# Optimization experiments

Measured on AMD Instinct MI355X. Metric: run time of the kernel, lower is better.

Reference implementation:

```python
import jax, jax.numpy as jnp
import numpy as np

L, M, B = 32768, 8, 8192      # lines, max neighbors per line, blocks
LIN, BIN, H = 768, 768, 512   # line_in_dim, block_in_dim, hidden_size
NH, DH = 8, 512 // 8          # heads, head_dim
LN_EPS = 1e-5


def _ln(x, g, b):
    mu = jnp.mean(x, axis=-1, keepdims=True)
    var = jnp.mean(jnp.square(x - mu), axis=-1, keepdims=True)
    return (x - mu) * jax.lax.rsqrt(var + LN_EPS) * g + b


def setup_inputs() -> dict:
    key = jax.random.key(0)
    ks = jax.random.split(key, 12)
    w = lambda k, shape, fan: jax.random.normal(k, shape, jnp.float32) * (fan ** -0.5)
    return {
        'global_lines': jax.random.normal(ks[0], (L, LIN), jnp.float32),
        'block_reprs': jax.random.normal(ks[1], (B, BIN), jnp.float32),
        'Wq': w(ks[2], (H, LIN), LIN),            # q_proj (no bias)
        'Wkv': w(ks[3], (H, BIN), BIN),           # kv_proj (no bias)
        'qn_g': jnp.ones((H,), jnp.float32), 'qn_b': jnp.zeros((H,), jnp.float32),
        'kvn_g': jnp.ones((H,), jnp.float32), 'kvn_b': jnp.zeros((H,), jnp.float32),
        'in_proj_w': w(ks[4], (3 * H, H), H), 'in_proj_b': jnp.zeros((3 * H,), jnp.float32),
        'out_w': w(ks[5], (H, H), H), 'out_b': jnp.zeros((H,), jnp.float32),
        'p1_w': w(ks[6], (H, 2 * H), 2 * H), 'p1_b': jnp.zeros((H,), jnp.float32),
        'ln1_g': jnp.ones((H,), jnp.float32), 'ln1_b': jnp.zeros((H,), jnp.float32),
        'p2_w': w(ks[7], (H, H), H), 'p2_b': jnp.zeros((H,), jnp.float32),
        'ln2_g': jnp.ones((H,), jnp.float32), 'ln2_b': jnp.zeros((H,), jnp.float32),
        'head_w': w(ks[8], (1, H), H), 'head_b': jnp.zeros((1,), jnp.float32),
        'K_indices': jax.random.randint(ks[9], (L, M), 0, B, jnp.int32),
        'neighbor_counts': jnp.clip(jax.random.randint(ks[10], (L,), 0, M + 1, jnp.int32), 1, M),
    }


def reference(global_lines, block_reprs, Wq, Wkv, qn_g, qn_b, kvn_g, kvn_b,
              in_proj_w, in_proj_b, out_w, out_b,
              p1_w, p1_b, ln1_g, ln1_b, p2_w, p2_b, ln2_g, ln2_b,
              head_w, head_b, K_indices, neighbor_counts):
    # q = LN(q_proj(lines))                              [L, H]
    q = _ln(global_lines @ Wq.T, qn_g, qn_b)
    # gather neighbor block reprs, project, LN           [L, M, H]
    kv = _ln(block_reprs[K_indices] @ Wkv.T, kvn_g, kvn_b)
    pad = jnp.arange(M)[None, :] >= neighbor_counts[:, None]  # True = padded key

    # torch nn.MultiheadAttention with query length 1 per line
    wq_i, wk_i, wv_i = jnp.split(in_proj_w, 3, axis=0)
    bq_i, bk_i, bv_i = jnp.split(in_proj_b, 3, axis=0)
    qh = (q @ wq_i.T + bq_i).reshape(L, NH, DH)
    kh = (kv @ wk_i.T + bk_i).reshape(L, M, NH, DH)
    vh = (kv @ wv_i.T + bv_i).reshape(L, M, NH, DH)
    scores = jnp.einsum('lhd,lmhd->lhm', qh, kh) / np.float32(np.sqrt(DH))
    scores = jnp.where(pad[:, None, :], jnp.finfo(scores.dtype).min, scores)
    attn = jax.nn.softmax(scores, axis=-1)
    ctx = jnp.einsum('lhm,lmhd->lhd', attn, vh).reshape(L, H)
    attn_out = ctx @ out_w.T + out_b

    # line_proj: Linear(2H->H) + LN + GELU + residual(Linear + LN + GELU)
    x = jnp.concatenate([q, attn_out], axis=-1)
    x = jax.nn.gelu(_ln(x @ p1_w.T + p1_b, ln1_g, ln1_b), approximate=False)
    x = x + jax.nn.gelu(_ln(x @ p2_w.T + p2_b, ln2_g, ln2_b), approximate=False)
    logits = (x @ head_w.T + head_b)[:, 0]
    return jax.nn.sigmoid(logits)
```

## Files before the change

### kernel.cpp

```cpp
#include <hip/hip_runtime.h>
#include <math.h>


typedef unsigned short u16;
typedef unsigned int u32;
using bf16x8 = __attribute__((ext_vector_type(8))) __bf16;
using u16x8  = __attribute__((ext_vector_type(8))) u16;
using f32x4  = __attribute__((ext_vector_type(4))) float;

__device__ __forceinline__ u16 f2bf(float f) {
    u32 u = __builtin_bit_cast(u32, f);
    u32 r = u + 0x7fffu + ((u >> 16) & 1u);
    return (u16)(r >> 16);
}
__device__ __forceinline__ float bf2f(u16 h) {
    return __builtin_bit_cast(float, (u32)h << 16);
}
__device__ __forceinline__ float gelu_exact(float x) {
    return 0.5f * x * (1.0f + erff(x * 0.70710678118654752440f));
}

__device__ __forceinline__ float breduce1(float s0, float* sm) {
    #pragma unroll
    for (int off = 32; off > 0; off >>= 1) s0 += __shfl_down(s0, off);
    const int lane = threadIdx.x & 63, w = threadIdx.x >> 6;
    __syncthreads();
    if (lane == 0) sm[w] = s0;
    __syncthreads();
    return sm[0] + sm[1] + sm[2] + sm[3];
}

__global__ __launch_bounds__(256) void cvt_bf16(
    const float* __restrict__ s, u16* __restrict__ d, int n)
{
    const int i = (blockIdx.x * 256 + threadIdx.x) * 4;
    if (i >= n) return;
    const float4 v = *reinterpret_cast<const float4*>(s + i);
    ushort4 o = make_ushort4(f2bf(v.x), f2bf(v.y), f2bf(v.z), f2bf(v.w));
    *reinterpret_cast<ushort4*>(d + i) = o;
}

struct CvtJobs {
    const float* s[5];
    u16* d[5];
    int cum[6];
};
__global__ __launch_bounds__(256) void cvt_multi(CvtJobs j)
{
    const int g = blockIdx.x * 256 + threadIdx.x;
    if (g >= j.cum[5]) return;
    int seg = 0;
    #pragma unroll
    for (int k = 1; k < 5; ++k) seg += (g >= j.cum[k]);
    const int q = g - j.cum[seg];
    const float4 v = *reinterpret_cast<const float4*>(j.s[seg] + q * 4);
    ushort4 o = make_ushort4(f2bf(v.x), f2bf(v.y), f2bf(v.z), f2bf(v.w));
    *reinterpret_cast<ushort4*>(j.d[seg] + q * 4) = o;
}

__global__ __launch_bounds__(256) void fold_w2(
    const float* __restrict__ p1w, const float* __restrict__ outw,
    u16* __restrict__ p1cb)
{
    __shared__ float As[16][65];
    __shared__ float Bs[16][65];
    const int tx = threadIdx.x & 15, ty = threadIdx.x >> 4;
    const int i0 = blockIdx.y * 64, j0 = blockIdx.x * 64;
    const int lr = threadIdx.x >> 2;
    const int lc = (threadIdx.x & 3) * 4;
    const int kr = threadIdx.x >> 4;
    const int jc = (threadIdx.x & 15) * 4;
    float acc[4][4] = {};
    for (int k0 = 0; k0 < 512; k0 += 16) {
        const float4 av = *reinterpret_cast<const float4*>(
            p1w + (size_t)(i0 + lr) * 1024 + 512 + k0 + lc);
        As[lc + 0][lr] = av.x; As[lc + 1][lr] = av.y;
        As[lc + 2][lr] = av.z; As[lc + 3][lr] = av.w;
        const float4 bv = *reinterpret_cast<const float4*>(
            outw + (size_t)(k0 + kr) * 512 + j0 + jc);
        Bs[kr][jc + 0] = bv.x; Bs[kr][jc + 1] = bv.y;
        Bs[kr][jc + 2] = bv.z; Bs[kr][jc + 3] = bv.w;
        __syncthreads();
        #pragma unroll
        for (int kk = 0; kk < 16; ++kk) {
            float a[4], b[4];
            #pragma unroll
            for (int i = 0; i < 4; ++i) a[i] = As[kk][ty * 4 + i];
            #pragma unroll
            for (int jj = 0; jj < 4; ++jj) b[jj] = Bs[kk][tx * 4 + jj];
            #pragma unroll
            for (int i = 0; i < 4; ++i)
                #pragma unroll
                for (int jj = 0; jj < 4; ++jj)
                    acc[i][jj] = fmaf(a[i], b[jj], acc[i][jj]);
        }
        __syncthreads();
    }
    #pragma unroll
    for (int i = 0; i < 4; ++i)
        #pragma unroll
        for (int jj = 0; jj < 4; ++jj)
            p1cb[(size_t)(i0 + ty * 4 + i) * 1024 + 512 + j0 + tx * 4 + jj] =
                f2bf(acc[i][jj]);
}

__global__ __launch_bounds__(64) void fold_bias(
    const float* __restrict__ p1w, const float* __restrict__ outb,
    const float* __restrict__ p1b, float* __restrict__ bias2)
{
    const int i = blockIdx.x, lane = threadIdx.x;
    float s = 0.0f;
    #pragma unroll
    for (int k = lane; k < 512; k += 64)
        s += p1w[(size_t)i * 1024 + 512 + k] * outb[k];
    #pragma unroll
    for (int off = 32; off > 0; off >>= 1) s += __shfl_down(s, off);
    if (lane == 0) bias2[i] = s + p1b[i];
}

template<bool HAS_A2, bool STATS>
__global__ __launch_bounds__(256) void gemm_bf16(
    const u16* __restrict__ A1, const u16* __restrict__ A2, int K1, int K,
    const u16* __restrict__ W, const float* __restrict__ bias,
    u16* __restrict__ C, int N, float* __restrict__ stats)
{
    __shared__ __bf16 As[128 * 32];
    __shared__ __bf16 Ws[128 * 32];
    const int tid = threadIdx.x;
    const int w = tid >> 6, lane = tid & 63;
    const int row0 = blockIdx.y * 128;
    const int col0 = blockIdx.x * 128;
    const int wr = (w >> 1) * 64, wc = (w & 1) * 64;
    const int fr = lane & 15, fg = lane >> 4;

    int srow[2], scol[2], soff[2];
    #pragma unroll
    for (int c = 0; c < 2; ++c) {
        const int bo = w * 2048 + c * 1024 + lane * 16;
        srow[c] = bo >> 6;
        scol[c] = (bo & 63) >> 1;
        soff[c] = (w * 2048 + c * 1024) >> 1;
    }

    f32x4 acc[4][4] = {};

    for (int k0 = 0; k0 < K; k0 += 32) {
        #pragma unroll
        for (int c = 0; c < 2; ++c) {
            const u16* asrc;
            if (HAS_A2) {
                const bool first = (k0 < K1);
                const u16* base = first ? A1 : A2;
                const int ldk = first ? K1 : (K - K1);
                const int kk  = first ? k0 : (k0 - K1);
                asrc = base + (size_t)(row0 + srow[c]) * ldk + kk + scol[c];
            } else {
                asrc = A1 + (size_t)(row0 + srow[c]) * K + k0 + scol[c];
            }
            __builtin_amdgcn_global_load_lds(
                (const __attribute__((address_space(1))) u32*)asrc,
                (__attribute__((address_space(3))) u32*)(As + soff[c]), 16, 0, 0);
            const u16* wsrc = W + (size_t)(col0 + srow[c]) * K + k0 + scol[c];
            __builtin_amdgcn_global_load_lds(
                (const __attribute__((address_space(1))) u32*)wsrc,
                (__attribute__((address_space(3))) u32*)(Ws + soff[c]), 16, 0, 0);
        }
        __syncthreads();

        bf16x8 af[4], bfr[4];
        #pragma unroll
        for (int m = 0; m < 4; ++m) {
            af[m]  = *(const bf16x8*)(As + (wr + m * 16 + fr) * 32 + fg * 8);
            bfr[m] = *(const bf16x8*)(Ws + (wc + m * 16 + fr) * 32 + fg * 8);
        }
        #pragma unroll
        for (int m = 0; m < 4; ++m)
            #pragma unroll
            for (int n = 0; n < 4; ++n)
                acc[m][n] = __builtin_amdgcn_mfma_f32_16x16x32_bf16(
                    af[m], bfr[n], acc[m][n], 0, 0, 0);
        __syncthreads();
    }

    if (bias) {
        #pragma unroll
        for (int n = 0; n < 4; ++n) {
            const float bv = bias[col0 + wc + n * 16 + fr];
            #pragma unroll
            for (int m = 0; m < 4; ++m)
                #pragma unroll
                for (int r = 0; r < 4; ++r)
                    acc[m][n][r] += bv;
        }
    }

    #pragma unroll
    for (int m = 0; m < 4; ++m)
        #pragma unroll
        for (int n = 0; n < 4; ++n) {
            const int col = col0 + wc + n * 16 + fr;
            #pragma unroll
            for (int r = 0; r < 4; ++r) {
                const int row = row0 + wr + m * 16 + fg * 4 + r;
                C[(size_t)row * N + col] = f2bf(acc[m][n][r]);
            }
        }

    if (STATS) {
        float ps[4][4], pq[4][4];
        #pragma unroll
        for (int m = 0; m < 4; ++m)
            #pragma unroll
            for (int r = 0; r < 4; ++r) {
                float s = 0.0f, q2 = 0.0f;
                #pragma unroll
                for (int n = 0; n < 4; ++n) {
                    const float v = acc[m][n][r];
                    s += v; q2 = fmaf(v, v, q2);
                }
                ps[m][r] = s; pq[m][r] = q2;
            }
        #pragma unroll
        for (int off = 1; off < 16; off <<= 1)
            #pragma unroll
            for (int m = 0; m < 4; ++m)
                #pragma unroll
                for (int r = 0; r < 4; ++r) {
                    ps[m][r] += __shfl_xor(ps[m][r], off);
                    pq[m][r] += __shfl_xor(pq[m][r], off);
                }
        if (fr == 0) {
            const int cb = blockIdx.x * 2 + (w & 1);
            #pragma unroll
            for (int m = 0; m < 4; ++m)
                #pragma unroll
                for (int r = 0; r < 4; ++r) {
                    const int row = row0 + wr + m * 16 + fg * 4 + r;
                    *reinterpret_cast<float2*>(stats + ((size_t)row * 8 + cb) * 2) =
                        make_float2(ps[m][r], pq[m][r]);
                }
        }
    }
}

template<bool GELU>
__global__ __launch_bounds__(256) void ln_rows_s(
    u16* __restrict__ X, const float* __restrict__ stats,
    const float* __restrict__ g, const float* __restrict__ b)
{
    const size_t row = blockIdx.x;
    float s = 0.0f, q2 = 0.0f;
    #pragma unroll
    for (int cb = 0; cb < 8; ++cb) {
        s  += stats[(row * 8 + cb) * 2];
        q2 += stats[(row * 8 + cb) * 2 + 1];
    }
    const float mu = s * (1.0f / 512.0f);
    const float var = q2 * (1.0f / 512.0f) - mu * mu;
    const float rs = rsqrtf(var + 1e-5f);
    const int t = threadIdx.x;
    const ushort2 xv = *reinterpret_cast<const ushort2*>(X + row * 512 + 2 * t);
    const float2 gg = *reinterpret_cast<const float2*>(g + 2 * t);
    const float2 bb = *reinterpret_cast<const float2*>(b + 2 * t);
    float y0 = (bf2f(xv.x) - mu) * rs * gg.x + bb.x;
    float y1 = (bf2f(xv.y) - mu) * rs * gg.y + bb.y;
    if (GELU) { y0 = gelu_exact(y0); y1 = gelu_exact(y1); }
    *reinterpret_cast<ushort2*>(X + row * 512 + 2 * t) = make_ushort2(f2bf(y0), f2bf(y1));
}

__global__ __launch_bounds__(512) void attn_kernel(
    const u16* __restrict__ qh, const u16* __restrict__ kvb,
    const int* __restrict__ kidx, const int* __restrict__ ncnt,
    u16* __restrict__ ctx)
{
    const int head = threadIdx.x >> 6;
    const int lane = threadIdx.x & 63;
    const int mi = lane & 7, dg = lane >> 3;
    const bool b0 = (mi & 1), b1 = (mi & 2), b2 = (mi & 4);
    const int doff = (b0 ? 4 : 0) + (b1 ? 2 : 0) + (b2 ? 1 : 0);

    for (int l = blockIdx.x; l < 32768; l += gridDim.x) {
        const int cnt = ncnt[l];
        const int idx = kidx[l * 8 + mi];
        const size_t kvbase = (size_t)idx * 1024 + head * 64 + dg * 8;

        const u16x8 qv = *(const u16x8*)(qh + (size_t)l * 512 + head * 64 + dg * 8);
        const u16x8 kv = *(const u16x8*)(kvb + kvbase);
        const u16x8 vv = *(const u16x8*)(kvb + kvbase + 512);

        float p = 0.0f;
        #pragma unroll
        for (int jj = 0; jj < 8; ++jj) p = fmaf(bf2f(qv[jj]), bf2f(kv[jj]), p);
        p += __shfl_xor(p, 8); p += __shfl_xor(p, 16); p += __shfl_xor(p, 32);

        float s = (mi < cnt) ? p * 0.125f : -3.402823466e38f;
        float mx = s;
        mx = fmaxf(mx, __shfl_xor(mx, 1));
        mx = fmaxf(mx, __shfl_xor(mx, 2));
        mx = fmaxf(mx, __shfl_xor(mx, 4));
        const float e = __expf(s - mx);
        float den = e;
        den += __shfl_xor(den, 1); den += __shfl_xor(den, 2); den += __shfl_xor(den, 4);
        const float wgt = e / den;

        float c[8];
        #pragma unroll
        for (int jj = 0; jj < 8; ++jj) c[jj] = wgt * bf2f(vv[jj]);

        #pragma unroll
        for (int jj = 0; jj < 4; ++jj) {
            const float snd = b0 ? c[jj] : c[jj + 4];
            const float rec = __shfl_xor(snd, 1);
            c[jj] = (b0 ? c[jj + 4] : c[jj]) + rec;
        }
        #pragma unroll
        for (int jj = 0; jj < 2; ++jj) {
            const float snd = b1 ? c[jj] : c[jj + 2];
            const float rec = __shfl_xor(snd, 2);
            c[jj] = (b1 ? c[jj + 2] : c[jj]) + rec;
        }
        {
            const float snd = b2 ? c[0] : c[1];
            const float rec = __shfl_xor(snd, 4);
            c[0] = (b2 ? c[1] : c[0]) + rec;
        }
        ctx[(size_t)l * 512 + head * 64 + dg * 8 + doff] = f2bf(c[0]);
    }
}

__global__ __launch_bounds__(256) void final_head_s(
    const u16* __restrict__ h1, const u16* __restrict__ h2raw,
    const float* __restrict__ stats,
    const float* __restrict__ g, const float* __restrict__ b,
    const float* __restrict__ hw, const float* __restrict__ hb,
    float* __restrict__ out)
{
    __shared__ float sm[4];
    const size_t row = blockIdx.x;
    float s = 0.0f, q2 = 0.0f;
    #pragma unroll
    for (int cb = 0; cb < 8; ++cb) {
        s  += stats[(row * 8 + cb) * 2];
        q2 += stats[(row * 8 + cb) * 2 + 1];
    }
    const float mu = s * (1.0f / 512.0f);
    const float var = q2 * (1.0f / 512.0f) - mu * mu;
    const float rs = rsqrtf(var + 1e-5f);
    const int t = threadIdx.x;
    const ushort2 xv = *reinterpret_cast<const ushort2*>(h2raw + row * 512 + 2 * t);
    const ushort2 hv = *reinterpret_cast<const ushort2*>(h1 + row * 512 + 2 * t);
    const float2 gg = *reinterpret_cast<const float2*>(g + 2 * t);
    const float2 bb = *reinterpret_cast<const float2*>(b + 2 * t);
    const float2 hwv = *reinterpret_cast<const float2*>(hw + 2 * t);
    const float y0 = bf2f(hv.x) + gelu_exact((bf2f(xv.x) - mu) * rs * gg.x + bb.x);
    const float y1 = bf2f(hv.y) + gelu_exact((bf2f(xv.y) - mu) * rs * gg.y + bb.y);
    const float d = breduce1(y0 * hwv.x + y1 * hwv.y, sm);
    if (t == 0) out[row] = 1.0f / (1.0f + expf(-(d + hb[0])));
}

extern "C" void kernel_launch(void* const* d_in, const int* in_sizes, int n_in,
                              void* d_out, int out_size, void* d_ws, size_t ws_size,
                              hipStream_t stream)
{
    const float* lines  = (const float*)d_in[0];
    const float* blocks = (const float*)d_in[1];
    const float* Wq     = (const float*)d_in[2];
    const float* Wkv    = (const float*)d_in[3];
    const float* qn_g   = (const float*)d_in[4];
    const float* qn_b   = (const float*)d_in[5];
    const float* kvn_g  = (const float*)d_in[6];
    const float* kvn_b  = (const float*)d_in[7];
    const float* in_w   = (const float*)d_in[8];
    const float* in_b   = (const float*)d_in[9];
    const float* out_w  = (const float*)d_in[10];
    const float* out_b  = (const float*)d_in[11];
    const float* p1_w   = (const float*)d_in[12];
    const float* p1_b   = (const float*)d_in[13];
    const float* ln1_g  = (const float*)d_in[14];
    const float* ln1_b  = (const float*)d_in[15];
    const float* p2_w   = (const float*)d_in[16];
    const float* p2_b   = (const float*)d_in[17];
    const float* ln2_g  = (const float*)d_in[18];
    const float* ln2_b  = (const float*)d_in[19];
    const float* head_w = (const float*)d_in[20];
    const float* head_b = (const float*)d_in[21];
    const int*   kidx   = (const int*)d_in[22];
    const int*   ncnt   = (const int*)d_in[23];
    float* out = (float*)d_out;

    char* wsb = (char*)d_ws;
    u16* qb    = (u16*)(wsb);
    u16* qhb   = (u16*)(wsb + (32ull << 20));
    u16* ctxb  = (u16*)(wsb + (64ull << 20));
    u16* kvbb  = (u16*)(wsb + (96ull << 20));
    u16* bkvb  = (u16*)(wsb + (112ull << 20));
    u16* Lb    = (u16*)(wsb + (120ull << 20));
    float* stats_h1 = (float*)(wsb + (120ull << 20));
    float* stats_h2 = (float*)(wsb + (124ull << 20));
    u16* Bb    = (u16*)(wsb + (168ull << 20));
    u16* Wqb   = (u16*)(wsb + (180ull << 20));
    u16* Wkvb  = Wqb + 512 * 768;
    u16* inwb  = Wkvb + 512 * 768;
    u16* p1cb  = inwb + 1536 * 512;
    u16* p2wb  = p1cb + 512 * 1024;
    float* stats_q   = (float*)(wsb + (185ull << 20));
    float* stats_bkv = (float*)(wsb + (187ull << 20));
    float* bias2f    = (float*)(wsb + (187ull << 20) + (512ull << 10));

    cvt_bf16<<<(32768 * 768 / 4 + 255) / 256, 256, 0, stream>>>(lines, Lb, 32768 * 768);
    cvt_bf16<<<(8192 * 768 / 4 + 255) / 256, 256, 0, stream>>>(blocks, Bb, 8192 * 768);
    {
        CvtJobs j;
        const float* ss[5] = { Wq, Wkv, in_w, p1_w, p2_w };
        u16* dd[5] = { Wqb, Wkvb, inwb, p1cb, p2wb };
        const int nn[5] = { 512 * 768, 512 * 768, 1536 * 512, 512 * 1024, 512 * 512 };
        int c = 0;
        for (int k = 0; k < 5; ++k) { j.s[k] = ss[k]; j.d[k] = dd[k]; j.cum[k] = c; c += nn[k] / 4; }
        j.cum[5] = c;
        cvt_multi<<<(c + 255) / 256, 256, 0, stream>>>(j);
    }
    fold_w2<<<dim3(8, 8), 256, 0, stream>>>(p1_w, out_w, p1cb);
    fold_bias<<<512, 64, 0, stream>>>(p1_w, out_b, p1_b, bias2f);

    gemm_bf16<false, true><<<dim3(4, 64), 256, 0, stream>>>(
        Bb, nullptr, 768, 768, Wkvb, nullptr, bkvb, 512, stats_bkv);
    ln_rows_s<false><<<8192, 256, 0, stream>>>(bkvb, stats_bkv, kvn_g, kvn_b);
    gemm_bf16<false, false><<<dim3(8, 64), 256, 0, stream>>>(
        bkvb, nullptr, 512, 512, inwb + 512 * 512, in_b + 512, kvbb, 1024, nullptr);
    gemm_bf16<false, true><<<dim3(4, 256), 256, 0, stream>>>(
        Lb, nullptr, 768, 768, Wqb, nullptr, qb, 512, stats_q);
    ln_rows_s<false><<<32768, 256, 0, stream>>>(qb, stats_q, qn_g, qn_b);
    gemm_bf16<false, false><<<dim3(4, 256), 256, 0, stream>>>(
        qb, nullptr, 512, 512, inwb, in_b, qhb, 512, nullptr);
    attn_kernel<<<2048, 512, 0, stream>>>(qhb, kvbb, kidx, ncnt, ctxb);
    gemm_bf16<true, true><<<dim3(4, 256), 256, 0, stream>>>(
        qb, ctxb, 512, 1024, p1cb, bias2f, qhb, 512, stats_h1);
    ln_rows_s<true><<<32768, 256, 0, stream>>>(qhb, stats_h1, ln1_g, ln1_b);
    gemm_bf16<false, true><<<dim3(4, 256), 256, 0, stream>>>(
        qhb, nullptr, 512, 512, p2wb, p2_b, ctxb, 512, stats_h2);
    final_head_s<<<32768, 256, 0, stream>>>(qhb, ctxb, stats_h2, ln2_g, ln2_b,
                                            head_w, head_b, out);
}
```

Measured before the change: 483.3 us.

## Fuse fp32-to-bf16 input conversion into projection GEMM loads and remap workgroups

Drops the two standalone conversion kernels for global_lines and block_reprs. The first-projection GEMMs now read fp32 A tiles directly, convert them in registers and store bf16 into LDS, which removes a full write and re-read of the converted activations. The A path for this mode switches from async global-to-LDS loads to synchronous register loads, which may reduce load overlap. It also adds an XCD-aware workgroup id remap to all GEMMs for better cache locality, and compacts the workspace layout.

Result: faster. 467.2 us (-3.3%).

```diff
diff --git a/kernel.cpp b/kernel.cpp
--- a/kernel.cpp
+++ b/kernel.cpp
@@ -28,16 +28,6 @@
     if (lane == 0) sm[w] = s0;
     __syncthreads();
     return sm[0] + sm[1] + sm[2] + sm[3];
-}
-
-__global__ __launch_bounds__(256) void cvt_bf16(
-    const float* __restrict__ s, u16* __restrict__ d, int n)
-{
-    const int i = (blockIdx.x * 256 + threadIdx.x) * 4;
-    if (i >= n) return;
-    const float4 v = *reinterpret_cast<const float4*>(s + i);
-    ushort4 o = make_ushort4(f2bf(v.x), f2bf(v.y), f2bf(v.z), f2bf(v.w));
-    *reinterpret_cast<ushort4*>(d + i) = o;
 }
 
 struct CvtJobs {
@@ -118,9 +108,9 @@
     if (lane == 0) bias2[i] = s + p1b[i];
 }
 
-template<bool HAS_A2, bool STATS>
+template<int A_MODE, bool STATS>
 __global__ __launch_bounds__(256) void gemm_bf16(
-    const u16* __restrict__ A1, const u16* __restrict__ A2, int K1, int K,
+    const void* __restrict__ A1v, const void* __restrict__ A2v, int K1, int K,
     const u16* __restrict__ W, const float* __restrict__ bias,
     u16* __restrict__ C, int N, float* __restrict__ stats)
 {
@@ -128,8 +118,15 @@
     __shared__ __bf16 Ws[128 * 32];
     const int tid = threadIdx.x;
     const int w = tid >> 6, lane = tid & 63;
-    const int row0 = blockIdx.y * 128;
-    const int col0 = blockIdx.x * 128;
+
+    const u32 nx = gridDim.x;
+    const u32 orig = blockIdx.y * nx + blockIdx.x;
+    const u32 nwg = nx * gridDim.y;
+    const u32 wgid = (orig & 7u) * (nwg >> 3) + (orig >> 3);
+    const int bx = wgid % nx;
+    const int row0 = (int)(wgid / nx) * 128;
+    const int col0 = bx * 128;
+
     const int wr = (w >> 1) * 64, wc = (w & 1) * 64;
     const int fr = lane & 15, fg = lane >> 4;
 
@@ -141,25 +138,46 @@
         scol[c] = (bo & 63) >> 1;
         soff[c] = (w * 2048 + c * 1024) >> 1;
     }
+    const int ar = tid >> 1;
+    const int ac = (tid & 1) * 16;
 
     f32x4 acc[4][4] = {};
 
     for (int k0 = 0; k0 < K; k0 += 32) {
+        if (A_MODE == 1) {
+            const float* Af = (const float*)A1v;
+            const float* src = Af + (size_t)(row0 + ar) * K + k0 + ac;
+            const float4 v0 = *reinterpret_cast<const float4*>(src);
+            const float4 v1 = *reinterpret_cast<const float4*>(src + 4);
+            const float4 v2 = *reinterpret_cast<const float4*>(src + 8);
+            const float4 v3 = *reinterpret_cast<const float4*>(src + 12);
+            u16x8 p0, p1;
+            p0[0] = f2bf(v0.x); p0[1] = f2bf(v0.y); p0[2] = f2bf(v0.z); p0[3] = f2bf(v0.w);
+            p0[4] = f2bf(v1.x); p0[5] = f2bf(v1.y); p0[6] = f2bf(v1.z); p0[7] = f2bf(v1.w);
+            p1[0] = f2bf(v2.x); p1[1] = f2bf(v2.y); p1[2] = f2bf(v2.z); p1[3] = f2bf(v2.w);
+            p1[4] = f2bf(v3.x); p1[5] = f2bf(v3.y); p1[6] = f2bf(v3.z); p1[7] = f2bf(v3.w);
+            *reinterpret_cast<u16x8*>((u16*)As + ar * 32 + ac) = p0;
+            *reinterpret_cast<u16x8*>((u16*)As + ar * 32 + ac + 8) = p1;
+        } else {
+            #pragma unroll
+            for (int c = 0; c < 2; ++c) {
+                const u16* asrc;
+                if (A_MODE == 2) {
+                    const bool first = (k0 < K1);
+                    const u16* base = first ? (const u16*)A1v : (const u16*)A2v;
+                    const int ldk = first ? K1 : (K - K1);
+                    const int kk  = first ? k0 : (k0 - K1);
+                    asrc = base + (size_t)(row0 + srow[c]) * ldk + kk + scol[c];
+                } else {
+                    asrc = (const u16*)A1v + (size_t)(row0 + srow[c]) * K + k0 + scol[c];
+                }
+                __builtin_amdgcn_global_load_lds(
+                    (const __attribute__((address_space(1))) u32*)asrc,
+                    (__attribute__((address_space(3))) u32*)(As + soff[c]), 16, 0, 0);
+            }
+        }
         #pragma unroll
         for (int c = 0; c < 2; ++c) {
-            const u16* asrc;
-            if (HAS_A2) {
-                const bool first = (k0 < K1);
-                const u16* base = first ? A1 : A2;
-                const int ldk = first ? K1 : (K - K1);
-                const int kk  = first ? k0 : (k0 - K1);
-                asrc = base + (size_t)(row0 + srow[c]) * ldk + kk + scol[c];
-            } else {
-                asrc = A1 + (size_t)(row0 + srow[c]) * K + k0 + scol[c];
-            }
-            __builtin_amdgcn_global_load_lds(
-                (const __attribute__((address_space(1))) u32*)asrc,
-                (__attribute__((address_space(3))) u32*)(As + soff[c]), 16, 0, 0);
             const u16* wsrc = W + (size_t)(col0 + srow[c]) * K + k0 + scol[c];
             __builtin_amdgcn_global_load_lds(
                 (const __attribute__((address_space(1))) u32*)wsrc,
@@ -230,7 +248,7 @@
                     pq[m][r] += __shfl_xor(pq[m][r], off);
                 }
         if (fr == 0) {
-            const int cb = blockIdx.x * 2 + (w & 1);
+            const int cb = bx * 2 + (w & 1);
             #pragma unroll
             for (int m = 0; m < 4; ++m)
                 #pragma unroll
@@ -394,21 +412,17 @@
     u16* ctxb  = (u16*)(wsb + (64ull << 20));
     u16* kvbb  = (u16*)(wsb + (96ull << 20));
     u16* bkvb  = (u16*)(wsb + (112ull << 20));
-    u16* Lb    = (u16*)(wsb + (120ull << 20));
-    float* stats_h1 = (float*)(wsb + (120ull << 20));
-    float* stats_h2 = (float*)(wsb + (124ull << 20));
-    u16* Bb    = (u16*)(wsb + (168ull << 20));
-    u16* Wqb   = (u16*)(wsb + (180ull << 20));
+    float* stats_q   = (float*)(wsb + (120ull << 20));
+    float* stats_h1  = (float*)(wsb + (124ull << 20));
+    float* stats_h2  = (float*)(wsb + (128ull << 20));
+    float* stats_bkv = (float*)(wsb + (132ull << 20));
+    u16* Wqb   = (u16*)(wsb + (136ull << 20));
     u16* Wkvb  = Wqb + 512 * 768;
     u16* inwb  = Wkvb + 512 * 768;
     u16* p1cb  = inwb + 1536 * 512;
     u16* p2wb  = p1cb + 512 * 1024;
-    float* stats_q   = (float*)(wsb + (185ull << 20));
-    float* stats_bkv = (float*)(wsb + (187ull << 20));
-    float* bias2f    = (float*)(wsb + (187ull << 20) + (512ull << 10));
-
-    cvt_bf16<<<(32768 * 768 / 4 + 255) / 256, 256, 0, stream>>>(lines, Lb, 32768 * 768);
-    cvt_bf16<<<(8192 * 768 / 4 + 255) / 256, 256, 0, stream>>>(blocks, Bb, 8192 * 768);
+    float* bias2f = (float*)(p2wb + 512 * 512);
+
     {
         CvtJobs j;
         const float* ss[5] = { Wq, Wkv, in_w, p1_w, p2_w };
@@ -422,21 +436,21 @@
     fold_w2<<<dim3(8, 8), 256, 0, stream>>>(p1_w, out_w, p1cb);
     fold_bias<<<512, 64, 0, stream>>>(p1_w, out_b, p1_b, bias2f);
 
-    gemm_bf16<false, true><<<dim3(4, 64), 256, 0, stream>>>(
-        Bb, nullptr, 768, 768, Wkvb, nullptr, bkvb, 512, stats_bkv);
+    gemm_bf16<1, true><<<dim3(4, 64), 256, 0, stream>>>(
+        blocks, nullptr, 768, 768, Wkvb, nullptr, bkvb, 512, stats_bkv);
     ln_rows_s<false><<<8192, 256, 0, stream>>>(bkvb, stats_bkv, kvn_g, kvn_b);
-    gemm_bf16<false, false><<<dim3(8, 64), 256, 0, stream>>>(
+    gemm_bf16<0, false><<<dim3(8, 64), 256, 0, stream>>>(
         bkvb, nullptr, 512, 512, inwb + 512 * 512, in_b + 512, kvbb, 1024, nullptr);
-    gemm_bf16<false, true><<<dim3(4, 256), 256, 0, stream>>>(
-        Lb, nullptr, 768, 768, Wqb, nullptr, qb, 512, stats_q);
+    gemm_bf16<1, true><<<dim3(4, 256), 256, 0, stream>>>(
+        lines, nullptr, 768, 768, Wqb, nullptr, qb, 512, stats_q);
     ln_rows_s<false><<<32768, 256, 0, stream>>>(qb, stats_q, qn_g, qn_b);
-    gemm_bf16<false, false><<<dim3(4, 256), 256, 0, stream>>>(
+    gemm_bf16<0, false><<<dim3(4, 256), 256, 0, stream>>>(
         qb, nullptr, 512, 512, inwb, in_b, qhb, 512, nullptr);
     attn_kernel<<<2048, 512, 0, stream>>>(qhb, kvbb, kidx, ncnt, ctxb);
-    gemm_bf16<true, true><<<dim3(4, 256), 256, 0, stream>>>(
+    gemm_bf16<2, true><<<dim3(4, 256), 256, 0, stream>>>(
         qb, ctxb, 512, 1024, p1cb, bias2f, qhb, 512, stats_h1);
     ln_rows_s<true><<<32768, 256, 0, stream>>>(qhb, stats_h1, ln1_g, ln1_b);
-    gemm_bf16<false, true><<<dim3(4, 256), 256, 0, stream>>>(
+    gemm_bf16<0, true><<<dim3(4, 256), 256, 0, stream>>>(
         qhb, nullptr, 512, 512, p2wb, p2_b, ctxb, 512, stats_h2);
     final_head_s<<<32768, 256, 0, stream>>>(qhb, ctxb, stats_h2, ln2_g, ln2_b,
                                             head_w, head_b, out);
```
